# Kernel tuning notes

Hardware: AMD Instinct MI355X
Metric: run time of the kernel (lower is better)

## Reference

```python
import jax, jax.numpy as jnp
import numpy as np

B, T, DIM = 2, 2048, 1024
H, DH, E, K = 16, 64, 8, 2


def setup_inputs() -> dict:
    key = jax.random.key(0)
    ks = jax.random.split(key, 7)
    s = 0.02
    return {
        "x":  jax.random.normal(ks[0], (B, T, DIM), jnp.float32),
        "Wq": jax.random.normal(ks[1], (H, DH, DIM), jnp.float32) * s,  # Linear(dim -> h*dh), reshaped
        "Wk": jax.random.normal(ks[2], (H, DH, DIM), jnp.float32) * s,
        "Wv": jax.random.normal(ks[3], (E, DH, DIM), jnp.float32) * s,  # per-expert Linear(dim -> dh)
        "Ws": jax.random.normal(ks[4], (H, E, DIM), jnp.float32) * s,   # V-gate Linear(dim -> h*e)
        "Wd": jax.random.normal(ks[5], (H, E, DIM), jnp.float32) * s,   # O-gate Linear(dim -> h*e)
        "Wo": jax.random.normal(ks[6], (E, DIM, DH), jnp.float32) * s,  # per-expert Linear(dh -> dim)
    }


def reference(x, Wq, Wk, Wv, Ws, Wd, Wo):
    scale = DH ** -0.5
    # projections: [b,h,t,dh]
    q = jnp.einsum('btc,hdc->bhtd', x, Wq)
    k = jnp.einsum('btc,hdc->bhtd', x, Wk)

    # ---- compute_moe (V experts): top-k gate, sigmoid weights ----
    gate_v = jnp.einsum('btc,hec->bthe', x, Ws)              # [b,t,h,e]
    w, sel = jax.lax.top_k(gate_v, K)                        # [b,t,h,K]
    wsig = jax.nn.sigmoid(w)
    oh = jax.nn.one_hot(sel, E, dtype=x.dtype)               # [b,t,h,K,e]
    mix_v = jnp.einsum('bthk,bthke->bthe', wsig, oh)         # weighted routing mask
    proj_v = jnp.einsum('btc,edc->bted', x, Wv)              # all-expert V projections (E small)
    v = jnp.einsum('bthe,bted->bhtd', mix_v, proj_v)         # [b,h,t,dh]

    # ---- standard attention core ----
    scores = jnp.einsum('bhid,bhjd->bhij', q * scale, k)     # [b,h,t,t]
    probs = jax.nn.softmax(scores, axis=-1)
    attn = jnp.einsum('bhij,bhjd->bihd', probs, v)           # [b,t,h,dh]

    # ---- compute_moe_o (O experts): top-k gate; NOTE original never uses its
    # softmax weights, so selected experts are summed UNWEIGHTED ----
    gate_o = jnp.einsum('btc,hec->bthe', x, Wd)
    _, sel_o = jax.lax.top_k(gate_o, K)
    mask_o = jax.nn.one_hot(sel_o, E, dtype=x.dtype).sum(axis=3)  # [b,t,h,e] in {0,1}
    res = jnp.einsum('bthe,bthd,efd->bthf', mask_o, attn, Wo)     # [b,t,h,dim]
    return res.sum(axis=2)                                        # [b,t,dim]
```

## Files before the change

kernel.cpp:

```cpp
#include <hip/hip_runtime.h>
#include <math.h>

#define TSEQ 2048
#define NB   2
#define NH   16
#define NE   8
#define DHD  64
#define MDIM 1024
#define MBT  4096
#define LDQKV 2560
#define GTAU 1e-3f
#define MAXFLAG 16384

typedef __attribute__((ext_vector_type(8))) short bf16x8;
typedef __attribute__((ext_vector_type(4))) float f32x4;
typedef __attribute__((ext_vector_type(16))) float f32x16;
typedef unsigned int u32;

__device__ inline unsigned short f2bf(float f) {
    union { float f; unsigned u; } v; v.f = f;
    unsigned r = v.u + 0x7fff + ((v.u >> 16) & 1);
    return (unsigned short)(r >> 16);
}
__device__ inline float bf2f(unsigned short h) {
    union { unsigned u; float f; } v; v.u = ((unsigned)h) << 16;
    return v.f;
}
__device__ inline u32 cvtpk(float a, float b) {
    u32 r;
    asm("v_cvt_pk_bf16_f32 %0, %1, %2" : "=v"(r) : "v"(a), "v"(b));
    return r;
}
__device__ inline float fexp2(float x) {
#if __has_builtin(__builtin_amdgcn_exp2f)
    return __builtin_amdgcn_exp2f(x);
#else
    float r; asm("v_exp_f32 %0, %1" : "=v"(r) : "v"(x)); return r;
#endif
}

__device__ inline void gload16(const void* g, void* l) {
    __builtin_amdgcn_global_load_lds((const __attribute__((address_space(1))) u32*)g,
                                     (__attribute__((address_space(3))) u32*)l, 16, 0, 0);
}

__device__ inline void cast8s(const float* __restrict__ in, unsigned short* __restrict__ out,
                              int i, float sc) {
    const float4* p = (const float4*)(in + (size_t)i * 8);
    float4 a = p[0], b = p[1];
    unsigned short o[8] = { f2bf(a.x*sc), f2bf(a.y*sc), f2bf(a.z*sc), f2bf(a.w*sc),
                            f2bf(b.x*sc), f2bf(b.y*sc), f2bf(b.z*sc), f2bf(b.w*sc) };
    *(uint4*)(out + (size_t)i * 8) = *(const uint4*)o;
}
__device__ inline void cast8hl(const float* __restrict__ in,
                               unsigned short* __restrict__ oh, unsigned short* __restrict__ ol,
                               int i) {
    const float4* p = (const float4*)(in + (size_t)i * 8);
    float4 a = p[0], b = p[1];
    float f[8] = { a.x, a.y, a.z, a.w, b.x, b.y, b.z, b.w };
    unsigned short h8[8], l8[8];
    #pragma unroll
    for (int j = 0; j < 8; ++j) {
        unsigned short hi = f2bf(f[j]);
        h8[j] = hi;
        l8[j] = f2bf(f[j] - bf2f(hi));
    }
    *(uint4*)(oh + (size_t)i * 8) = *(const uint4*)h8;
    *(uint4*)(ol + (size_t)i * 8) = *(const uint4*)l8;
}

__global__ __launch_bounds__(256)
void prep(const float* __restrict__ x,  const float* __restrict__ Wq,
          const float* __restrict__ Wk, const float* __restrict__ Wv,
          const float* __restrict__ Ws, const float* __restrict__ Wd,
          const float* __restrict__ Wo,
          unsigned short* __restrict__ xb, unsigned short* __restrict__ xbl,
          unsigned short* __restrict__ Wqkvb,
          unsigned short* __restrict__ Wsdh, unsigned short* __restrict__ Wsdl,
          unsigned short* __restrict__ WoTh, unsigned short* __restrict__ WoTl,
          u32* __restrict__ flags)
{
    const float qsc = 0.125f * 1.4426950408889634f;
    int b = blockIdx.x, tid = threadIdx.x;
    if (b == 0 && tid == 0) flags[0] = 0;
    if (b < 2048)      cast8hl(x, xb, xbl,          (b        ) * 256 + tid);
    else if (b < 2560) cast8s(Wq, Wqkvb,            (b - 2048) * 256 + tid, qsc);
    else if (b < 3072) cast8s(Wk, Wqkvb + 1048576,  (b - 2560) * 256 + tid, 1.f);
    else if (b < 3328) cast8s(Wv, Wqkvb + 2097152,  (b - 3072) * 256 + tid, 1.f);
    else if (b < 3456) {
        int i = (b - 3328) * 256 + tid;
        const float* src = (i < 16384) ? Ws + (size_t)i * 8 : Wd + (size_t)(i - 16384) * 8;
        const float4* p = (const float4*)src;
        float4 a = p[0], bq = p[1];
        float f8[8] = { a.x, a.y, a.z, a.w, bq.x, bq.y, bq.z, bq.w };
        unsigned short h8[8], l8[8];
        #pragma unroll
        for (int j = 0; j < 8; ++j) {
            unsigned short hi = f2bf(f8[j]);
            h8[j] = hi;
            l8[j] = f2bf(f8[j] - bf2f(hi));
        }
        *(uint4*)(Wsdh + (size_t)i * 8) = *(const uint4*)h8;
        *(uint4*)(Wsdl + (size_t)i * 8) = *(const uint4*)l8;
    } else {
        int idx = (b - 3456) * 256 + tid;
        int f = idx >> 9, ed = idx & 511, e = ed >> 6, d = ed & 63;
        float v = Wo[(size_t)e * (MDIM * DHD) + (size_t)f * DHD + d];
        unsigned short hi = f2bf(v);
        WoTh[idx] = hi;
        WoTl[idx] = f2bf(v - bf2f(hi));
    }
}

__global__ __launch_bounds__(256)
void qkvgate(const unsigned short* __restrict__ A,
             const unsigned short* __restrict__ B,
             unsigned short* __restrict__ C,
             const unsigned short* __restrict__ Al,
             const unsigned short* __restrict__ Bh2, const unsigned short* __restrict__ Bl2,
             float2* __restrict__ wv, u32* __restrict__ selv, u32* __restrict__ selo,
             u32* __restrict__ flags)
{
    __shared__ __align__(16) unsigned short S[8192];
    const int tid = threadIdx.x;
    const int lane = tid & 63, wave = tid >> 6;
    const int fr = lane & 15, fg = lane >> 4;
    const int grow = lane >> 2, gcol = (lane & 3) * 8;

    if (blockIdx.x < 640) {
        const int K = 1024, N = LDQKV, nbx = 20;
        unsigned short* As = S;
        unsigned short* Bs = S + 4096;
        const int o = blockIdx.x;
        const int virt = (o & 7) * 80 + (o >> 3);
        const int bx = virt % nbx, by = virt / nbx;
        const int m0 = by * 128, n0 = bx * 128;
        const int wm = (wave >> 1) * 64, wn = (wave & 1) * 64;

        f32x4 acc[4][4];
        #pragma unroll
        for (int i = 0; i < 4; ++i)
            #pragma unroll
            for (int j = 0; j < 4; ++j) acc[i][j] = (f32x4)0.f;

        for (int k0 = 0; k0 < K; k0 += 32) {
            __syncthreads();
            const unsigned short* gA = A + (size_t)(m0 + wave * 32 + grow) * K + k0 + gcol;
            gload16(gA,                  As + wave * 1024);
            gload16(gA + (size_t)16 * K, As + wave * 1024 + 512);
            const unsigned short* gB = B + (size_t)(n0 + wave * 32 + grow) * K + k0 + gcol;
            gload16(gB,                  Bs + wave * 1024);
            gload16(gB + (size_t)16 * K, Bs + wave * 1024 + 512);
            __syncthreads();
            bf16x8 af[4], bfr[4];
            #pragma unroll
            for (int t = 0; t < 4; ++t) {
                af[t]  = *(const bf16x8*)(As + (wm + t * 16 + fr) * 32 + fg * 8);
                bfr[t] = *(const bf16x8*)(Bs + (wn + t * 16 + fr) * 32 + fg * 8);
            }
            #pragma unroll
            for (int i = 0; i < 4; ++i)
                #pragma unroll
                for (int j = 0; j < 4; ++j)
                    acc[i][j] = __builtin_amdgcn_mfma_f32_16x16x32_bf16(af[i], bfr[j], acc[i][j], 0, 0, 0);
        }
        #pragma unroll
        for (int i = 0; i < 4; ++i)
            #pragma unroll
            for (int j = 0; j < 4; ++j)
                #pragma unroll
                for (int rr = 0; rr < 4; ++rr) {
                    int row = m0 + wm + i * 16 + fg * 4 + rr;
                    int col = n0 + wn + j * 16 + fr;
                    C[(size_t)row * N + col] = f2bf(acc[i][j][rr]);
                }
    } else {
        const int K = 1024;
        const int g = blockIdx.x - 640;
        const int m0 = (g >> 2) * 64, n0 = (g & 3) * 64;
        const int wm = (wave >> 1) * 32, wn = (wave & 1) * 32;
        const unsigned short* src = (wave == 0) ? A : (wave == 1) ? Al : (wave == 2) ? Bh2 : Bl2;
        const int brow = (wave >= 2) ? n0 : m0;

        f32x4 acc[2][2];
        #pragma unroll
        for (int i = 0; i < 2; ++i)
            #pragma unroll
            for (int j = 0; j < 2; ++j) acc[i][j] = (f32x4)0.f;

        for (int k0 = 0; k0 < K; k0 += 32) {
            __syncthreads();
            #pragma unroll
            for (int i = 0; i < 4; ++i)
                gload16(src + (size_t)(brow + i * 16 + grow) * K + k0 + gcol,
                        S + wave * 2048 + i * 512);
            __syncthreads();
            bf16x8 ah[2], al[2], bh[2], bl[2];
            #pragma unroll
            for (int t = 0; t < 2; ++t) {
                ah[t] = *(const bf16x8*)(S +        (wm + t * 16 + fr) * 32 + fg * 8);
                al[t] = *(const bf16x8*)(S + 2048 + (wm + t * 16 + fr) * 32 + fg * 8);
                bh[t] = *(const bf16x8*)(S + 4096 + (wn + t * 16 + fr) * 32 + fg * 8);
                bl[t] = *(const bf16x8*)(S + 6144 + (wn + t * 16 + fr) * 32 + fg * 8);
            }
            #pragma unroll
            for (int i = 0; i < 2; ++i)
                #pragma unroll
                for (int j = 0; j < 2; ++j) {
                    acc[i][j] = __builtin_amdgcn_mfma_f32_16x16x32_bf16(ah[i], bh[j], acc[i][j], 0, 0, 0);
                    acc[i][j] = __builtin_amdgcn_mfma_f32_16x16x32_bf16(ah[i], bl[j], acc[i][j], 0, 0, 0);
                    acc[i][j] = __builtin_amdgcn_mfma_f32_16x16x32_bf16(al[i], bh[j], acc[i][j], 0, 0, 0);
                }
        }
        float* Tf = (float*)S;
        __syncthreads();
        #pragma unroll
        for (int i = 0; i < 2; ++i)
            #pragma unroll
            for (int j = 0; j < 2; ++j)
                #pragma unroll
                for (int rr = 0; rr < 4; ++rr)
                    Tf[(wm + i * 16 + fg * 4 + rr) * 64 + wn + j * 16 + fr] = acc[i][j][rr];
        __syncthreads();
        const int type = (n0 >= 128);
        const int hbase = (n0 & 127) >> 3;
        #pragma unroll
        for (int k = 0; k < 2; ++k) {
            int it = tid + k * 256;
            int lr = it >> 3, lh = it & 7;
            int item = (m0 + lr) * 16 + hbase + lh;
            const float* gp = Tf + lr * 64 + lh * 8;
            float b1 = -1e30f, b2 = -1e30f, b3 = -1e30f; int e1 = 0, e2 = 0;
            #pragma unroll
            for (int e = 0; e < NE; ++e) {
                float v = gp[e];
                if (v > b1)      { b3 = b2; b2 = b1; e2 = e1; b1 = v; e1 = e; }
                else if (v > b2) { b3 = b2; b2 = v;  e2 = e; }
                else if (v > b3) { b3 = v; }
            }
            if (type == 0) {
                wv[item] = make_float2(1.f / (1.f + __expf(-b1)), 1.f / (1.f + __expf(-b2)));
                selv[item] = (u32)e1 | ((u32)e2 << 4);
                if (b2 - b3 < GTAU) {
                    u32 p = atomicAdd(flags, 1u);
                    if (p < MAXFLAG) flags[1 + p] = (u32)item;
                }
            } else {
                selo[item] = (1u << e1) | (1u << e2);
                if (b2 - b3 < GTAU) {
                    u32 p = atomicAdd(flags, 1u);
                    if (p < MAXFLAG) flags[1 + p] = (u32)item | 0x10000u;
                }
            }
        }
    }
}

__global__ __launch_bounds__(256)
void mfma_gemm3(const unsigned short* __restrict__ Ah, const unsigned short* __restrict__ Al,
                const unsigned short* __restrict__ Bh, const unsigned short* __restrict__ Bl,
                float* __restrict__ C)
{
    const int Kc = 512, N = 1024;
    __shared__ __align__(16) unsigned short Ash[128 * 32];
    __shared__ __align__(16) unsigned short Asl[128 * 32];
    __shared__ __align__(16) unsigned short Bsh[64 * 32];
    __shared__ __align__(16) unsigned short Bsl[64 * 32];
    const int o = blockIdx.x;
    const int virt = (o & 7) * 64 + (o >> 3);
    const int bx = virt & 15, by = virt >> 4;
    const int tid = threadIdx.x;
    const int lane = tid & 63, wave = tid >> 6;
    const int m0 = by * 128, n0 = bx * 64;
    const int wm = (wave >> 1) * 64, wn = (wave & 1) * 32;
    const int fr = lane & 15, fg = lane >> 4;
    const int grow = lane >> 2, gcol = (lane & 3) * 8;

    f32x4 acc[4][2];
    #pragma unroll
    for (int i = 0; i < 4; ++i)
        #pragma unroll
        for (int j = 0; j < 2; ++j) acc[i][j] = (f32x4)0.f;

    for (int k0 = 0; k0 < Kc; k0 += 32) {
        __syncthreads();
        const size_t roff  = (size_t)(m0 + wave * 32 + grow) * Kc + k0 + gcol;
        const size_t roffB = (size_t)(n0 + wave * 16 + grow) * Kc + k0 + gcol;
        gload16(Ah + roff,             Ash + wave * 1024);
        gload16(Ah + roff + 16 * Kc,   Ash + wave * 1024 + 512);
        gload16(Al + roff,             Asl + wave * 1024);
        gload16(Al + roff + 16 * Kc,   Asl + wave * 1024 + 512);
        gload16(Bh + roffB,            Bsh + wave * 512);
        gload16(Bl + roffB,            Bsl + wave * 512);
        __syncthreads();
        bf16x8 ah[4], al[4], bh[2], bl[2];
        #pragma unroll
        for (int t = 0; t < 4; ++t) {
            ah[t] = *(const bf16x8*)(Ash + (wm + t * 16 + fr) * 32 + fg * 8);
            al[t] = *(const bf16x8*)(Asl + (wm + t * 16 + fr) * 32 + fg * 8);
        }
        #pragma unroll
        for (int t = 0; t < 2; ++t) {
            bh[t] = *(const bf16x8*)(Bsh + (wn + t * 16 + fr) * 32 + fg * 8);
            bl[t] = *(const bf16x8*)(Bsl + (wn + t * 16 + fr) * 32 + fg * 8);
        }
        #pragma unroll
        for (int i = 0; i < 4; ++i)
            #pragma unroll
            for (int j = 0; j < 2; ++j) {
                acc[i][j] = __builtin_amdgcn_mfma_f32_16x16x32_bf16(ah[i], bh[j], acc[i][j], 0, 0, 0);
                acc[i][j] = __builtin_amdgcn_mfma_f32_16x16x32_bf16(ah[i], bl[j], acc[i][j], 0, 0, 0);
                acc[i][j] = __builtin_amdgcn_mfma_f32_16x16x32_bf16(al[i], bh[j], acc[i][j], 0, 0, 0);
            }
    }
    #pragma unroll
    for (int i = 0; i < 4; ++i)
        #pragma unroll
        for (int j = 0; j < 2; ++j)
            #pragma unroll
            for (int rr = 0; rr < 4; ++rr) {
                int row = m0 + wm + i * 16 + fg * 4 + rr;
                int col = n0 + wn + j * 16 + fr;
                C[(size_t)row * N + col] = acc[i][j][rr];
            }
}

__global__ __launch_bounds__(256)
void gate_fix(const float* __restrict__ x, const float* __restrict__ Ws,
              const float* __restrict__ Wd, const u32* __restrict__ flags,
              float2* __restrict__ wv, u32* __restrict__ selv, u32* __restrict__ selo)
{
    u32 nf = flags[0]; if (nf > MAXFLAG) nf = MAXFLAG;
    int gw = (blockIdx.x * 256 + threadIdx.x) >> 6;
    int lane = threadIdx.x & 63;
    int nwaves = gridDim.x * 4;
    for (u32 w = gw; w < nf; w += nwaves) {
        u32 rec = flags[1 + w];
        int item = rec & 0xffff, which = rec >> 16;
        int bt = item >> 4, h = item & 15;
        const float* W = (which ? Wd : Ws) + (size_t)h * NE * MDIM + lane * 16;
        const float* xr = x + (size_t)bt * MDIM + lane * 16;
        double g[8];
        #pragma unroll
        for (int e = 0; e < 8; ++e) {
            double s = 0.0;
            #pragma unroll
            for (int c = 0; c < 16; ++c)
                s += (double)xr[c] * (double)W[(size_t)e * MDIM + c];
            g[e] = s;
        }
        #pragma unroll
        for (int off = 32; off; off >>= 1)
            #pragma unroll
            for (int e = 0; e < 8; ++e)
                g[e] += __shfl_xor(g[e], off, 64);
        if (lane == 0) {
            double b1 = -1e300, b2 = -1e300; int i1 = 0, i2 = 0;
            #pragma unroll
            for (int e = 0; e < 8; ++e) {
                double v = g[e];
                if (v > b1)      { b2 = b1; i2 = i1; b1 = v; i1 = e; }
                else if (v > b2) { b2 = v;  i2 = e; }
            }
            if (which == 0) {
                wv[item] = make_float2(1.f / (1.f + __expf(-(float)b1)),
                                       1.f / (1.f + __expf(-(float)b2)));
                selv[item] = (u32)i1 | ((u32)i2 << 4);
            } else {
                selo[item] = (1u << i1) | (1u << i2);
            }
        }
    }
}

#define VTP 72
__global__ __launch_bounds__(256)
void vtrans(const unsigned short* __restrict__ QKVb, const float2* __restrict__ wv,
            const u32* __restrict__ selv, unsigned short* __restrict__ Vtg)
{
    __shared__ __align__(16) unsigned short Ls[256 * VTP];
    const int vid = blockIdx.x;
    const int xcd = vid & 7, local = vid >> 3;
    const int virt = xcd * 32 + local;
    const int b = virt >> 7, rem = virt & 127;
    const int tblk = rem >> 4, h = rem & 15;
    const int tid = threadIdx.x;

    {
        const int bt = b * TSEQ + tblk * 256 + tid;
        u32 s = selv[bt * 16 + h];
        float2 w = wv[bt * 16 + h];
        int e1 = s & 15, e2 = (s >> 4) & 15;
        const unsigned short* pv = QKVb + (size_t)bt * LDQKV + 2048;
        #pragma unroll
        for (int c = 0; c < 8; ++c) {
            uint4 a  = *(const uint4*)(pv + e1 * 64 + c * 8);
            uint4 bb = *(const uint4*)(pv + e2 * 64 + c * 8);
            unsigned short ea[8], eb[8], eo[8];
            *(uint4*)ea = a; *(uint4*)eb = bb;
            #pragma unroll
            for (int j = 0; j < 8; ++j)
                eo[j] = f2bf(w.x * bf2f(ea[j]) + w.y * bf2f(eb[j]));
            *(uint4*)(Ls + tid * VTP + c * 8) = *(const uint4*)eo;
        }
    }
    __syncthreads();
    {
        const int d = tid & 63, outer = tid >> 6;
        const size_t vrow = ((size_t)((b * NH + h) * DHD + d)) * TSEQ + tblk * 256;
        #pragma unroll
        for (int c8 = 0; c8 < 8; ++c8) {
            int t0 = (outer * 8 + c8) * 8;
            unsigned short o[8];
            #pragma unroll
            for (int j = 0; j < 8; ++j)
                o[j] = Ls[(t0 + j) * VTP + d];
            *(uint4*)(Vtg + vrow + t0) = *(const uint4*)o;
        }
    }
}

#define SPA 72
#define MFMA32(A,B,C) __builtin_amdgcn_mfma_f32_32x32x16_bf16(A, B, C, 0, 0, 0)
__global__ __launch_bounds__(256)
void attn_mfma(const unsigned short* __restrict__ QKVb,
               const unsigned short* __restrict__ Vtg,
               float* __restrict__ Op0, float* __restrict__ Op1,
               float* __restrict__ lp)
{
    __shared__ __align__(16) unsigned short Ks[64 * SPA];
    __shared__ __align__(16) unsigned short Vt[64 * SPA];
    const int vid = blockIdx.x;
    const int xcd = vid & 7, sl = vid >> 3;
    const int grp = xcd * 8 + (sl >> 4);
    const int q0  = (sl & 15) * 128;
    const int h   = grp & 15;
    const int z   = grp >> 4;
    const int b = z >> 1, split = z & 1;
    const int tid = threadIdx.x;
    const int lane = tid & 63, wq = tid >> 6;
    const int ql = lane & 31;
    const int hi = lane >> 5;
    const size_t base_q = ((size_t)b * TSEQ) * LDQKV + h * DHD;
    const size_t base_k = base_q + 1024;
    const size_t base_v = ((size_t)(b * NH + h) * DHD) * TSEQ;
    const int k00 = split * 1024;

    const int qrow = q0 + wq * 32 + ql;
    bf16x8 qa[4];
    #pragma unroll
    for (int t = 0; t < 4; ++t)
        qa[t] = *(const bf16x8*)(QKVb + base_q + (size_t)qrow * LDQKV + t * 16 + hi * 8);

    f32x16 o0 = (f32x16)0.f, o1 = (f32x16)0.f;
    float l_lane = 0.f;

    const int srow = tid >> 2, scol = (tid & 3) * 8;
    uint4 kr0 = *(const uint4*)(QKVb + base_k + (size_t)(k00 + srow) * LDQKV + scol);
    uint4 kr1 = *(const uint4*)(QKVb + base_k + (size_t)(k00 + srow) * LDQKV + scol + 32);
    uint4 vr0 = *(const uint4*)(Vtg + base_v + (size_t)srow * TSEQ + k00 + scol);
    uint4 vr1 = *(const uint4*)(Vtg + base_v + (size_t)srow * TSEQ + k00 + scol + 32);

    const int NT = 1024 / 64;
    for (int kb = 0; kb < NT; ++kb) {
        __syncthreads();
        *(uint4*)(Ks + srow * SPA + scol)      = kr0;
        *(uint4*)(Ks + srow * SPA + scol + 32) = kr1;
        *(uint4*)(Vt + srow * SPA + scol)      = vr0;
        *(uint4*)(Vt + srow * SPA + scol + 32) = vr1;
        __syncthreads();
        if (kb + 1 < NT) {
            const size_t gk = base_k + (size_t)(k00 + (kb + 1) * 64 + srow) * LDQKV + scol;
            const size_t gv = base_v + (size_t)srow * TSEQ + k00 + (kb + 1) * 64 + scol;
            kr0 = *(const uint4*)(QKVb + gk);
            kr1 = *(const uint4*)(QKVb + gk + 32);
            vr0 = *(const uint4*)(Vtg + gv);
            vr1 = *(const uint4*)(Vtg + gv + 32);
        }
        f32x16 s0 = (f32x16)0.f, s1 = (f32x16)0.f;
        #pragma unroll
        for (int t = 0; t < 4; ++t) {
            bf16x8 k0 = *(const bf16x8*)(Ks + ql * SPA + t * 16 + hi * 8);
            bf16x8 k1 = *(const bf16x8*)(Ks + (32 + ql) * SPA + t * 16 + hi * 8);
            s0 = MFMA32(k0, qa[t], s0);
            s1 = MFMA32(k1, qa[t], s1);
        }
        float ls0 = 0.f, ls1 = 0.f;
        u32 w[8];
        #pragma unroll
        for (int r = 0; r < 16; r += 2) {
            float pa = fexp2(s0[r]), pb = fexp2(s0[r + 1]);
            s0[r] = pa; s0[r + 1] = pb;
            ls0 += pa; ls1 += pb;
        }
        #pragma unroll
        for (int m = 0; m < 8; ++m) w[m] = cvtpk(s0[2*m], s0[2*m+1]);
        #pragma unroll
        for (int tl = 0; tl < 2; ++tl) {
            const int mb = 4 * tl, tk = tl;
            u32 a0 = w[mb],     b0 = w[mb + 2];
            u32 a1 = w[mb + 1], b1 = w[mb + 3];
            asm("v_permlane32_swap_b32 %0, %1" : "+v"(a0), "+v"(b0));
            asm("v_permlane32_swap_b32 %0, %1" : "+v"(a1), "+v"(b1));
            union { u32 uw[4]; bf16x8 v; } pu;
            pu.uw[0] = a0; pu.uw[1] = a1; pu.uw[2] = b0; pu.uw[3] = b1;
            bf16x8 v0 = *(const bf16x8*)(Vt + ql * SPA + tk * 16 + hi * 8);
            bf16x8 v1 = *(const bf16x8*)(Vt + (32 + ql) * SPA + tk * 16 + hi * 8);
            o0 = MFMA32(pu.v, v0, o0);
            o1 = MFMA32(pu.v, v1, o1);
        }
        #pragma unroll
        for (int r = 0; r < 16; r += 2) {
            float pa = fexp2(s1[r]), pb = fexp2(s1[r + 1]);
            s1[r] = pa; s1[r + 1] = pb;
            ls0 += pa; ls1 += pb;
        }
        #pragma unroll
        for (int m = 0; m < 8; ++m) w[m] = cvtpk(s1[2*m], s1[2*m+1]);
        #pragma unroll
        for (int tl = 0; tl < 2; ++tl) {
            const int mb = 4 * tl, tk = 2 + tl;
            u32 a0 = w[mb],     b0 = w[mb + 2];
            u32 a1 = w[mb + 1], b1 = w[mb + 3];
            asm("v_permlane32_swap_b32 %0, %1" : "+v"(a0), "+v"(b0));
            asm("v_permlane32_swap_b32 %0, %1" : "+v"(a1), "+v"(b1));
            union { u32 uw[4]; bf16x8 v; } pu;
            pu.uw[0] = a0; pu.uw[1] = a1; pu.uw[2] = b0; pu.uw[3] = b1;
            bf16x8 v0 = *(const bf16x8*)(Vt + ql * SPA + tk * 16 + hi * 8);
            bf16x8 v1 = *(const bf16x8*)(Vt + (32 + ql) * SPA + tk * 16 + hi * 8);
            o0 = MFMA32(pu.v, v0, o0);
            o1 = MFMA32(pu.v, v1, o1);
        }
        l_lane += ls0 + ls1;
    }
    float l_tot = l_lane + __shfl_xor(l_lane, 32, 64);
    float* Op = split ? Op1 : Op0;
    const size_t ob = ((size_t)b * TSEQ) * MDIM + h * DHD;
    #pragma unroll
    for (int r = 0; r < 16; ++r) {
        int qr = q0 + wq * 32 + (r & 3) + 8 * (r >> 2) + 4 * hi;
        Op[ob + (size_t)qr * MDIM + ql]      = o0[r];
        Op[ob + (size_t)qr * MDIM + 32 + ql] = o1[r];
    }
    if (hi == 0)
        lp[(((size_t)split * NB + b) * NH + h) * TSEQ + q0 + wq * 32 + ql] = l_tot;
}

__global__ __launch_bounds__(256)
void compute_U2(const float* __restrict__ Op0, const float* __restrict__ Op1,
                const float* __restrict__ lp, const u32* __restrict__ selo,
                unsigned short* __restrict__ Uh, unsigned short* __restrict__ Ul)
{
    int t = blockIdx.x * 256 + threadIdx.x;
    int bt = t >> 6, d = t & 63;
    int b = bt >> 11, ts = bt & 2047;
    float att[16];
    #pragma unroll
    for (int h = 0; h < NH; ++h) {
        size_t li = ((size_t)b * NH + h) * TSEQ + ts;
        float l = lp[li] + lp[li + (size_t)NB * NH * TSEQ];
        size_t oi = (size_t)bt * MDIM + h * DHD + d;
        att[h] = (Op0[oi] + Op1[oi]) / l;
    }
    const u32* sp = selo + bt * 16;
    u32 m[16];
    #pragma unroll
    for (int h = 0; h < NH; ++h) m[h] = sp[h];
    #pragma unroll
    for (int e = 0; e < NE; ++e) {
        float sum = 0.f;
        #pragma unroll
        for (int h = 0; h < NH; ++h)
            if (m[h] & (1u << e)) sum += att[h];
        int idx = bt * 512 + e * 64 + d;
        unsigned short hi16 = f2bf(sum);
        Uh[idx] = hi16;
        Ul[idx] = f2bf(sum - bf2f(hi16));
    }
}

extern "C" void kernel_launch(void* const* d_in, const int* in_sizes, int n_in,
                              void* d_out, int out_size, void* d_ws, size_t ws_size,
                              hipStream_t stream)
{
    const float* x  = (const float*)d_in[0];
    const float* Wq = (const float*)d_in[1];
    const float* Wk = (const float*)d_in[2];
    const float* Wv = (const float*)d_in[3];
    const float* Ws = (const float*)d_in[4];
    const float* Wd = (const float*)d_in[5];
    const float* Wo = (const float*)d_in[6];
    float* out = (float*)d_out;
    char* ws = (char*)d_ws;

    unsigned short* xb    = (unsigned short*)(ws);
    unsigned short* Wqkvb = (unsigned short*)(ws + 8388608);
    float*          Op0   = (float*)(ws);
    unsigned short* QKVb  = (unsigned short*)(ws + 16777216);
    unsigned short* Vtg   = (unsigned short*)(ws + 37748736);
    unsigned short* xbl   = (unsigned short*)(ws + 46137344);
    float*          Op1   = (float*)(ws + 46137344);
    float*          lp    = (float*)(ws + 62914560);
    unsigned short* WoTh  = (unsigned short*)(ws + 63438848);
    unsigned short* WoTl  = (unsigned short*)(ws + 64487424);
    unsigned short* Uh    = (unsigned short*)(ws + 65536000);
    u32*            flags = (u32*)(ws + 69730304);
    unsigned short* Ul    = (unsigned short*)(ws + 69730304);
    float2*         wvp   = (float2*)(ws + 73924608);
    u32*            selv  = (u32*)(ws + 74448896);
    u32*            selo  = (u32*)(ws + 74711040);
    unsigned short* Wsdh  = (unsigned short*)(ws + 74973184);
    unsigned short* Wsdl  = (unsigned short*)(ws + 75497472);

    dim3 blk(256);
    prep<<<5504, blk, 0, stream>>>(x, Wq, Wk, Wv, Ws, Wd, Wo,
                                   xb, xbl, Wqkvb, Wsdh, Wsdl, WoTh, WoTl, flags);

    qkvgate<<<896, blk, 0, stream>>>(xb, Wqkvb, QKVb, xbl, Wsdh, Wsdl,
                                     wvp, selv, selo, flags);

    gate_fix<<<128, blk, 0, stream>>>(x, Ws, Wd, flags, wvp, selv, selo);

    vtrans<<<256, blk, 0, stream>>>(QKVb, wvp, selv, Vtg);

    attn_mfma<<<1024, blk, 0, stream>>>(QKVb, Vtg, Op0, Op1, lp);

    compute_U2<<<1024, blk, 0, stream>>>(Op0, Op1, lp, selo, Uh, Ul);
    mfma_gemm3<<<512, blk, 0, stream>>>(Uh, Ul, WoTh, WoTl, out);
}
```

Before: 152.8 us.

## Swizzle LDS column layout in GEMMs and remap QKV tiles per XCD

Applies an XOR swizzle to the column chunk each lane loads from global memory into LDS, and applies the matching XOR on the fragment reads, in both the QKV/gate GEMM and the split-bf16 output GEMM. The goal is to remove LDS bank conflicts on the 16-byte fragment reads, where rows are 64 bytes apart. It also changes the QKV block-to-tile mapping so each XCD gets a contiguous 8x10 tile region, aiming for better L2 reuse of the A and B panels. Correctness depends on the write-side and read-side swizzles matching exactly.

```diff
diff --git a/kernel.cpp b/kernel.cpp
--- a/kernel.cpp
+++ b/kernel.cpp
@@ -128,14 +128,18 @@
     const int grow = lane >> 2, gcol = (lane & 3) * 8;
 
     if (blockIdx.x < 640) {
-        const int K = 1024, N = LDQKV, nbx = 20;
+        const int K = 1024, N = LDQKV;
         unsigned short* As = S;
         unsigned short* Bs = S + 4096;
         const int o = blockIdx.x;
-        const int virt = (o & 7) * 80 + (o >> 3);
-        const int bx = virt % nbx, by = virt / nbx;
+        const int xcd = o & 7, local = o >> 3;
+        const int lby = local / 10, lbx = local - lby * 10;
+        const int by = (xcd >> 1) * 8 + lby;
+        const int bx = (xcd & 1) * 10 + lbx;
         const int m0 = by * 128, n0 = bx * 128;
         const int wm = (wave >> 1) * 64, wn = (wave & 1) * 64;
+        const int swzcol = ((lane & 3) ^ ((lane >> 3) & 3)) * 8;
+        const int rsw = ((fr >> 1) & 3);
 
         f32x4 acc[4][4];
         #pragma unroll
@@ -145,18 +149,18 @@
 
         for (int k0 = 0; k0 < K; k0 += 32) {
             __syncthreads();
-            const unsigned short* gA = A + (size_t)(m0 + wave * 32 + grow) * K + k0 + gcol;
+            const unsigned short* gA = A + (size_t)(m0 + wave * 32 + grow) * K + k0 + swzcol;
             gload16(gA,                  As + wave * 1024);
             gload16(gA + (size_t)16 * K, As + wave * 1024 + 512);
-            const unsigned short* gB = B + (size_t)(n0 + wave * 32 + grow) * K + k0 + gcol;
+            const unsigned short* gB = B + (size_t)(n0 + wave * 32 + grow) * K + k0 + swzcol;
             gload16(gB,                  Bs + wave * 1024);
             gload16(gB + (size_t)16 * K, Bs + wave * 1024 + 512);
             __syncthreads();
             bf16x8 af[4], bfr[4];
             #pragma unroll
             for (int t = 0; t < 4; ++t) {
-                af[t]  = *(const bf16x8*)(As + (wm + t * 16 + fr) * 32 + fg * 8);
-                bfr[t] = *(const bf16x8*)(Bs + (wn + t * 16 + fr) * 32 + fg * 8);
+                af[t]  = *(const bf16x8*)(As + (wm + t * 16 + fr) * 32 + (fg ^ rsw) * 8);
+                bfr[t] = *(const bf16x8*)(Bs + (wn + t * 16 + fr) * 32 + (fg ^ rsw) * 8);
             }
             #pragma unroll
             for (int i = 0; i < 4; ++i)
@@ -274,7 +278,9 @@
     const int m0 = by * 128, n0 = bx * 64;
     const int wm = (wave >> 1) * 64, wn = (wave & 1) * 32;
     const int fr = lane & 15, fg = lane >> 4;
-    const int grow = lane >> 2, gcol = (lane & 3) * 8;
+    const int grow = lane >> 2;
+    const int swzcol = ((lane & 3) ^ ((lane >> 3) & 3)) * 8;
+    const int rsw = ((fr >> 1) & 3);
 
     f32x4 acc[4][2];
     #pragma unroll
@@ -284,8 +290,8 @@
 
     for (int k0 = 0; k0 < Kc; k0 += 32) {
         __syncthreads();
-        const size_t roff  = (size_t)(m0 + wave * 32 + grow) * Kc + k0 + gcol;
-        const size_t roffB = (size_t)(n0 + wave * 16 + grow) * Kc + k0 + gcol;
+        const size_t roff  = (size_t)(m0 + wave * 32 + grow) * Kc + k0 + swzcol;
+        const size_t roffB = (size_t)(n0 + wave * 16 + grow) * Kc + k0 + swzcol;
         gload16(Ah + roff,             Ash + wave * 1024);
         gload16(Ah + roff + 16 * Kc,   Ash + wave * 1024 + 512);
         gload16(Al + roff,             Asl + wave * 1024);
@@ -296,13 +302,13 @@
         bf16x8 ah[4], al[4], bh[2], bl[2];
         #pragma unroll
         for (int t = 0; t < 4; ++t) {
-            ah[t] = *(const bf16x8*)(Ash + (wm + t * 16 + fr) * 32 + fg * 8);
-            al[t] = *(const bf16x8*)(Asl + (wm + t * 16 + fr) * 32 + fg * 8);
+            ah[t] = *(const bf16x8*)(Ash + (wm + t * 16 + fr) * 32 + (fg ^ rsw) * 8);
+            al[t] = *(const bf16x8*)(Asl + (wm + t * 16 + fr) * 32 + (fg ^ rsw) * 8);
         }
         #pragma unroll
         for (int t = 0; t < 2; ++t) {
-            bh[t] = *(const bf16x8*)(Bsh + (wn + t * 16 + fr) * 32 + fg * 8);
-            bl[t] = *(const bf16x8*)(Bsl + (wn + t * 16 + fr) * 32 + fg * 8);
+            bh[t] = *(const bf16x8*)(Bsh + (wn + t * 16 + fr) * 32 + (fg ^ rsw) * 8);
+            bl[t] = *(const bf16x8*)(Bsl + (wn + t * 16 + fr) * 32 + (fg ^ rsw) * 8);
         }
         #pragma unroll
         for (int i = 0; i < 4; ++i)
```

New measurement: 151.4 us. About the same (-0.9%).
